# Optimization experiments

Measured on AMD Instinct MI355X. Metric: run time of the kernel, lower is better.

## Reference

```python
import jax, jax.numpy as jnp
import numpy as np

UNITS, D_IN, K_CONN, BATCH = 1024, 2048, 16, 4096
TEMP = 1.0  # temperature_update_tf at step=0 (epoch 0)
EPS = 1e-20


def setup_inputs() -> dict:
    key = jax.random.key(0)
    kx, kw, kd, kg = jax.random.split(key, 4)
    x = jax.random.normal(kx, (BATCH, D_IN), dtype=jnp.float32)
    # he_uniform for W
    limit = np.sqrt(6.0 / D_IN).astype(np.float32)
    W = jax.random.uniform(kw, (UNITS, D_IN), minval=-limit, maxval=limit, dtype=jnp.float32)
    # logits D ~ N(0, 0.5)
    D = 0.5 * jax.random.normal(kd, (UNITS, D_IN), dtype=jnp.float32)
    # Gumbel noise, scaled by -0.001 as in the original (BS=1)
    u = jax.random.uniform(kg, (1, UNITS, D_IN), dtype=jnp.float32)
    GN = -0.001 * jnp.log(-jnp.log(u + EPS) + EPS)
    return {"x": x, "W": W, "D": D, "GN": GN, "k": K_CONN}


def _hard_sigmoid(v):
    return jnp.clip(0.2 * v + 0.5, 0.0, 1.0)


def reference(x, W, D, GN, k):
    logits = D  # [units, d]
    perturbed = logits[None, :, :] + GN  # [1, units, d]
    # top-k indices, then sorted ascending (TF: top_k of indices + reverse)
    _, idx = jax.lax.top_k(perturbed, k)           # [1, units, k]
    idx_sorted = jnp.sort(idx, axis=-1)             # ascending index order
    hard = jax.nn.one_hot(idx_sorted, D_IN, dtype=perturbed.dtype)  # [1, units, k, d]
    # exclusive cumsum over the k axis
    cum = jnp.cumsum(hard, axis=-2) - hard
    # softmax((log(exp(logits)*(1-cum+eps)) + GN)/Temp) == softmax((logits + log(1-cum+eps) + GN)/Temp)
    scores = (logits[None, :, None, :] + jnp.log(1.0 - cum + EPS) + GN[:, :, None, :]) / TEMP
    soft = jax.nn.softmax(scores, axis=-1)          # [1, units, k, d]
    samples = jax.lax.stop_gradient(hard - soft) + soft
    A = samples.sum(axis=-2).sum(axis=0)            # [units, d]
    # straight-through binary weights
    w_soft = 2.0 * _hard_sigmoid(W) - 1.0
    w_bin = jax.lax.stop_gradient(jnp.sign(W) - w_soft) + w_soft
    AW = A * w_bin                                   # [units, d]
    y = x @ AW.T                                     # [batch, units]
    return y
```

## Files before the change

kernel.cpp:

```cpp
#include <hip/hip_runtime.h>
#include <hip/hip_bf16.h>

#define UNITS 1024
#define DIN   2048
#define KCONN 16
#define BATCH 4096
#define BB    8

__global__ __launch_bounds__(256) void topk_sel_kernel(
    const float* __restrict__ Dl, const float* __restrict__ GN,
    const float* __restrict__ W, int* __restrict__ selCi,
    float* __restrict__ selC) {
  __shared__ float P[4][DIN];
  __shared__ int chosen[4][KCONN];
  const int lane = threadIdx.x & 63;
  const int wv   = threadIdx.x >> 6;
  const int u    = blockIdx.x * 4 + wv;

  const float4* D4 = (const float4*)(Dl + (size_t)u * DIN);
  const float4* G4 = (const float4*)(GN + (size_t)u * DIN);
  float4* P4 = (float4*)P[wv];
#pragma unroll
  for (int i = 0; i < DIN / 4 / 64; ++i) {
    int e = i * 64 + lane;
    float4 d = D4[e], g = G4[e];
    P4[e] = make_float4(d.x + g.x, d.y + g.y, d.z + g.z, d.w + g.w);
  }
  __syncthreads();

  for (int it = 0; it < KCONN; ++it) {
    float best = -INFINITY;
    int   bi   = 0;
#pragma unroll
    for (int i = 0; i < DIN / 64; ++i) {
      float v = P[wv][i * 64 + lane];
      if (v > best) { best = v; bi = i * 64 + lane; }
    }
    unsigned b  = __float_as_uint(best);
    unsigned kv = b ^ (((int)b < 0) ? 0xFFFFFFFFu : 0x80000000u);
    int id = bi;
#define DSTEP(CTRL, RM) { \
    unsigned kv2 = (unsigned)__builtin_amdgcn_update_dpp((int)kv, (int)kv, CTRL, RM, 0xF, false); \
    int id2 = __builtin_amdgcn_update_dpp(id, id, CTRL, RM, 0xF, false); \
    bool tk = (kv2 > kv) || ((kv2 == kv) && (id2 < id)); \
    kv = tk ? kv2 : kv; id = tk ? id2 : id; }
    DSTEP(0x111, 0xF)
    DSTEP(0x112, 0xF)
    DSTEP(0x114, 0xF)
    DSTEP(0x118, 0xF)
    DSTEP(0x142, 0xA)
    DSTEP(0x143, 0xC)
#undef DSTEP
    int widx = __builtin_amdgcn_readlane(id, 63);
    if (lane == (widx & 63)) P[wv][widx] = -INFINITY;
    if (lane == 0) chosen[wv][it] = widx;
  }

  if (lane < KCONN) {
    int gi = chosen[wv][lane];
    float w = W[(size_t)u * DIN + gi];
    float c = (w > 0.0f) ? 1.0f : ((w < 0.0f) ? -1.0f : 0.0f);
    selCi[u * KCONN + lane] = gi ^ ((gi >> 3) & 7);
    selC[u * KCONN + lane]  = c;
  }
}

__global__ __launch_bounds__(512) void gather_mm_kernel(
    const float* __restrict__ x, const int* __restrict__ selCi,
    const float* __restrict__ selC, float* __restrict__ y) {
  __shared__ uint4 xs[DIN];
  const int t = threadIdx.x;
  const size_t b0 = (size_t)blockIdx.x * BB;

  const int4*   Ia = (const int4*)(selCi + t * KCONN);
  const int4*   Ib = (const int4*)(selCi + (t + 512) * KCONN);
  const float4* Ca = (const float4*)(selC + t * KCONN);
  const float4* Cb = (const float4*)(selC + (t + 512) * KCONN);
  int4   i0 = Ia[0], i1 = Ia[1], i2 = Ia[2], i3 = Ia[3];
  int4   i4 = Ib[0], i5 = Ib[1], i6 = Ib[2], i7 = Ib[3];
  float4 c0 = Ca[0], c1 = Ca[1], c2 = Ca[2], c3 = Ca[3];
  float4 c4 = Cb[0], c5 = Cb[1], c6 = Cb[2], c7 = Cb[3];

  const float* xb = x + b0 * DIN + 4 * t;
  float4 r0 = *(const float4*)(xb + 0 * DIN);
  float4 r1 = *(const float4*)(xb + 1 * DIN);
  float4 r2 = *(const float4*)(xb + 2 * DIN);
  float4 r3 = *(const float4*)(xb + 3 * DIN);
  float4 r4 = *(const float4*)(xb + 4 * DIN);
  float4 r5 = *(const float4*)(xb + 5 * DIN);
  float4 r6 = *(const float4*)(xb + 6 * DIN);
  float4 r7 = *(const float4*)(xb + 7 * DIN);

#define PK2(LO, HI) ({ __hip_bfloat16 l_ = __float2bfloat16(LO), h_ = __float2bfloat16(HI); \
  (unsigned)(*(unsigned short*)&l_) | ((unsigned)(*(unsigned short*)&h_) << 16); })
#define MKCH(J, C) { const int d_ = 4 * t + (J); const int sd_ = d_ ^ ((d_ >> 3) & 7); \
  uint4 ch_; ch_.x = PK2(r0.C, r1.C); ch_.y = PK2(r2.C, r3.C); \
  ch_.z = PK2(r4.C, r5.C); ch_.w = PK2(r6.C, r7.C); xs[sd_] = ch_; }
  MKCH(0, x) MKCH(1, y) MKCH(2, z) MKCH(3, w)
#undef MKCH
#undef PK2
  __syncthreads();

#define BL(w) __uint_as_float((w) << 16)
#define BH(w) __uint_as_float((w) & 0xffff0000u)
#define GJ(CI, CC) { uint4 v_ = xs[CI]; const float cc_ = (CC); \
  a0 = fmaf(cc_, BL(v_.x), a0); a1 = fmaf(cc_, BH(v_.x), a1); \
  a2 = fmaf(cc_, BL(v_.y), a2); a3 = fmaf(cc_, BH(v_.y), a3); \
  a4 = fmaf(cc_, BL(v_.z), a4); a5 = fmaf(cc_, BH(v_.z), a5); \
  a6 = fmaf(cc_, BL(v_.w), a6); a7 = fmaf(cc_, BH(v_.w), a7); }
#define UNIT(IA, IB, IC, ID, CA, CB, CC_, CD, U) { \
  float a0 = 0, a1 = 0, a2 = 0, a3 = 0, a4 = 0, a5 = 0, a6 = 0, a7 = 0; \
  GJ(IA.x, CA.x) GJ(IA.y, CA.y) GJ(IA.z, CA.z) GJ(IA.w, CA.w) \
  GJ(IB.x, CB.x) GJ(IB.y, CB.y) GJ(IB.z, CB.z) GJ(IB.w, CB.w) \
  GJ(IC.x, CC_.x) GJ(IC.y, CC_.y) GJ(IC.z, CC_.z) GJ(IC.w, CC_.w) \
  GJ(ID.x, CD.x) GJ(ID.y, CD.y) GJ(ID.z, CD.z) GJ(ID.w, CD.w) \
  const int u_ = (U); \
  y[(b0 + 0) * UNITS + u_] = a0; y[(b0 + 1) * UNITS + u_] = a1; \
  y[(b0 + 2) * UNITS + u_] = a2; y[(b0 + 3) * UNITS + u_] = a3; \
  y[(b0 + 4) * UNITS + u_] = a4; y[(b0 + 5) * UNITS + u_] = a5; \
  y[(b0 + 6) * UNITS + u_] = a6; y[(b0 + 7) * UNITS + u_] = a7; }

  UNIT(i0, i1, i2, i3, c0, c1, c2, c3, t)
  UNIT(i4, i5, i6, i7, c4, c5, c6, c7, t + 512)
#undef UNIT
#undef GJ
#undef BL
#undef BH
}

extern "C" void kernel_launch(void* const* d_in, const int* in_sizes, int n_in,
                              void* d_out, int out_size, void* d_ws, size_t ws_size,
                              hipStream_t stream) {
  const float* x  = (const float*)d_in[0];
  const float* W  = (const float*)d_in[1];
  const float* Dl = (const float*)d_in[2];
  const float* GN = (const float*)d_in[3];
  float* y = (float*)d_out;

  int*   selCi = (int*)d_ws;
  float* selC  = (float*)((char*)d_ws + UNITS * KCONN * sizeof(int));

  topk_sel_kernel<<<UNITS / 4, 256, 0, stream>>>(Dl, GN, W, selCi, selC);
  gather_mm_kernel<<<BATCH / BB, 512, 0, stream>>>(x, selCi, selC, y);
}
```

Before: 32.71 us.

## Register-resident top-k with per-lane top-2 cache and sign-packed gather indices

The top-k kernel now keeps each lane's 32 perturbed logits in registers and caches a per-lane top-2. This replaces the per-iteration full LDS rescan, and a lane only rescans its registers when both cached candidates are consumed. The selection output packs the swizzled column index and the sign bit of W into one int, with a zero-row sentinel for w==0. The gather kernel therefore loads half the metadata and applies the sign by XOR instead of an FMA. Nontemporal loads and stores are added for the streamed x, D, GN and y traffic.

```diff
diff --git a/kernel.cpp b/kernel.cpp
--- a/kernel.cpp
+++ b/kernel.cpp
@@ -7,43 +7,60 @@
 #define BATCH 4096
 #define BB    8
 
+typedef float    f32x4 __attribute__((ext_vector_type(4)));
+typedef unsigned u32x4 __attribute__((ext_vector_type(4)));
+typedef int      i32x4 __attribute__((ext_vector_type(4)));
+
+#define LDNT4F(P) __builtin_nontemporal_load((const f32x4*)(P))
+
 __global__ __launch_bounds__(256) void topk_sel_kernel(
     const float* __restrict__ Dl, const float* __restrict__ GN,
-    const float* __restrict__ W, int* __restrict__ selCi,
-    float* __restrict__ selC) {
-  __shared__ float P[4][DIN];
-  __shared__ int chosen[4][KCONN];
+    const float* __restrict__ W, int* __restrict__ selP) {
   const int lane = threadIdx.x & 63;
   const int wv   = threadIdx.x >> 6;
   const int u    = blockIdx.x * 4 + wv;
 
-  const float4* D4 = (const float4*)(Dl + (size_t)u * DIN);
-  const float4* G4 = (const float4*)(GN + (size_t)u * DIN);
-  float4* P4 = (float4*)P[wv];
+  const f32x4* D4 = (const f32x4*)(Dl + (size_t)u * DIN);
+  const f32x4* G4 = (const f32x4*)(GN + (size_t)u * DIN);
+  float v[32];
 #pragma unroll
-  for (int i = 0; i < DIN / 4 / 64; ++i) {
-    int e = i * 64 + lane;
-    float4 d = D4[e], g = G4[e];
-    P4[e] = make_float4(d.x + g.x, d.y + g.y, d.z + g.z, d.w + g.w);
+  for (int i4 = 0; i4 < 8; ++i4) {
+    f32x4 d = LDNT4F(D4 + i4 * 64 + lane);
+    f32x4 g = LDNT4F(G4 + i4 * 64 + lane);
+    v[i4 * 4 + 0] = d[0] + g[0];
+    v[i4 * 4 + 1] = d[1] + g[1];
+    v[i4 * 4 + 2] = d[2] + g[2];
+    v[i4 * 4 + 3] = d[3] + g[3];
   }
-  __syncthreads();
 
+  float m1 = -INFINITY, m2 = -INFINITY;
+  int   l1 = 0, l2 = 0;
+#pragma unroll
+  for (int l = 0; l < 32; ++l) {
+    float xv = v[l];
+    bool g1t = xv > m1;
+    bool g2t = xv > m2;
+    m2 = g1t ? m1 : (g2t ? xv : m2);
+    l2 = g1t ? l1 : (g2t ? l : l2);
+    m1 = g1t ? xv : m1;
+    l1 = g1t ? l  : l1;
+  }
+
+  unsigned claimed = 0;
+  int navail = 2;
+  int gsel = 0;
+
+#pragma unroll 1
   for (int it = 0; it < KCONN; ++it) {
-    float best = -INFINITY;
-    int   bi   = 0;
-#pragma unroll
-    for (int i = 0; i < DIN / 64; ++i) {
-      float v = P[wv][i * 64 + lane];
-      if (v > best) { best = v; bi = i * 64 + lane; }
-    }
-    unsigned b  = __float_as_uint(best);
-    unsigned kv = b ^ (((int)b < 0) ? 0xFFFFFFFFu : 0x80000000u);
-    int id = bi;
+    unsigned kb = __float_as_uint(m1);
+    unsigned kv = kb ^ (((int)kb < 0) ? 0xFFFFFFFFu : 0x80000000u);
+    int g1 = ((l1 >> 2) << 8) | (lane << 2) | (l1 & 3);
+    unsigned rk = kv; int rg = g1;
 #define DSTEP(CTRL, RM) { \
-    unsigned kv2 = (unsigned)__builtin_amdgcn_update_dpp((int)kv, (int)kv, CTRL, RM, 0xF, false); \
-    int id2 = __builtin_amdgcn_update_dpp(id, id, CTRL, RM, 0xF, false); \
-    bool tk = (kv2 > kv) || ((kv2 == kv) && (id2 < id)); \
-    kv = tk ? kv2 : kv; id = tk ? id2 : id; }
+    unsigned k2_ = (unsigned)__builtin_amdgcn_update_dpp((int)rk, (int)rk, CTRL, RM, 0xF, false); \
+    int g2_ = __builtin_amdgcn_update_dpp(rg, rg, CTRL, RM, 0xF, false); \
+    bool tk_ = (k2_ > rk) || ((k2_ == rk) && (g2_ < rg)); \
+    rk = tk_ ? k2_ : rk; rg = tk_ ? g2_ : rg; }
     DSTEP(0x111, 0xF)
     DSTEP(0x112, 0xF)
     DSTEP(0x114, 0xF)
@@ -51,81 +68,102 @@
     DSTEP(0x142, 0xA)
     DSTEP(0x143, 0xC)
 #undef DSTEP
-    int widx = __builtin_amdgcn_readlane(id, 63);
-    if (lane == (widx & 63)) P[wv][widx] = -INFINITY;
-    if (lane == 0) chosen[wv][it] = widx;
+    int wg = __builtin_amdgcn_readlane(rg, 63);
+    if (lane == it) gsel = wg;
+
+    bool own  = (g1 == wg);
+    bool need = own && (navail == 1);
+    if (own) claimed |= 1u << l1;
+    if (own && navail == 2) { m1 = m2; l1 = l2; navail = 1; }
+    if (need) {
+      float bm = -INFINITY; int bl = 0;
+#pragma unroll
+      for (int l = 0; l < 32; ++l) {
+        float xv = (claimed & (1u << l)) ? -INFINITY : v[l];
+        if (xv > bm) { bm = xv; bl = l; }
+      }
+      m1 = bm; l1 = bl;
+    }
   }
 
   if (lane < KCONN) {
-    int gi = chosen[wv][lane];
-    float w = W[(size_t)u * DIN + gi];
-    float c = (w > 0.0f) ? 1.0f : ((w < 0.0f) ? -1.0f : 0.0f);
-    selCi[u * KCONN + lane] = gi ^ ((gi >> 3) & 7);
-    selC[u * KCONN + lane]  = c;
+    int g = gsel;
+    float w = W[(size_t)u * DIN + g];
+    int sd = g ^ ((g >> 3) & 7);
+    int pa = (w == 0.0f) ? (DIN << 1)
+                         : ((sd << 1) | (w < 0.0f ? 1 : 0));
+    selP[u * KCONN + lane] = pa;
   }
 }
 
 __global__ __launch_bounds__(512) void gather_mm_kernel(
-    const float* __restrict__ x, const int* __restrict__ selCi,
-    const float* __restrict__ selC, float* __restrict__ y) {
-  __shared__ uint4 xs[DIN];
+    const float* __restrict__ x, const int* __restrict__ selP,
+    float* __restrict__ y) {
+  __shared__ u32x4 xs[DIN + 1];
   const int t = threadIdx.x;
   const size_t b0 = (size_t)blockIdx.x * BB;
 
-  const int4*   Ia = (const int4*)(selCi + t * KCONN);
-  const int4*   Ib = (const int4*)(selCi + (t + 512) * KCONN);
-  const float4* Ca = (const float4*)(selC + t * KCONN);
-  const float4* Cb = (const float4*)(selC + (t + 512) * KCONN);
-  int4   i0 = Ia[0], i1 = Ia[1], i2 = Ia[2], i3 = Ia[3];
-  int4   i4 = Ib[0], i5 = Ib[1], i6 = Ib[2], i7 = Ib[3];
-  float4 c0 = Ca[0], c1 = Ca[1], c2 = Ca[2], c3 = Ca[3];
-  float4 c4 = Cb[0], c5 = Cb[1], c6 = Cb[2], c7 = Cb[3];
+  const i32x4* S0 = (const i32x4*)(selP + t * KCONN);
+  const i32x4* S1 = (const i32x4*)(selP + (t + 512) * KCONN);
+  i32x4 sA0 = S0[0], sA1 = S0[1], sA2 = S0[2], sA3 = S0[3];
+  i32x4 sB0 = S1[0], sB1 = S1[1], sB2 = S1[2], sB3 = S1[3];
 
   const float* xb = x + b0 * DIN + 4 * t;
-  float4 r0 = *(const float4*)(xb + 0 * DIN);
-  float4 r1 = *(const float4*)(xb + 1 * DIN);
-  float4 r2 = *(const float4*)(xb + 2 * DIN);
-  float4 r3 = *(const float4*)(xb + 3 * DIN);
-  float4 r4 = *(const float4*)(xb + 4 * DIN);
-  float4 r5 = *(const float4*)(xb + 5 * DIN);
-  float4 r6 = *(const float4*)(xb + 6 * DIN);
-  float4 r7 = *(const float4*)(xb + 7 * DIN);
+  f32x4 r0 = LDNT4F(xb + 0 * DIN);
+  f32x4 r1 = LDNT4F(xb + 1 * DIN);
+  f32x4 r2 = LDNT4F(xb + 2 * DIN);
+  f32x4 r3 = LDNT4F(xb + 3 * DIN);
+  f32x4 r4 = LDNT4F(xb + 4 * DIN);
+  f32x4 r5 = LDNT4F(xb + 5 * DIN);
+  f32x4 r6 = LDNT4F(xb + 6 * DIN);
+  f32x4 r7 = LDNT4F(xb + 7 * DIN);
 
 #define PK2(LO, HI) ({ __hip_bfloat16 l_ = __float2bfloat16(LO), h_ = __float2bfloat16(HI); \
   (unsigned)(*(unsigned short*)&l_) | ((unsigned)(*(unsigned short*)&h_) << 16); })
-#define MKCH(J, C) { const int d_ = 4 * t + (J); const int sd_ = d_ ^ ((d_ >> 3) & 7); \
-  uint4 ch_; ch_.x = PK2(r0.C, r1.C); ch_.y = PK2(r2.C, r3.C); \
-  ch_.z = PK2(r4.C, r5.C); ch_.w = PK2(r6.C, r7.C); xs[sd_] = ch_; }
-  MKCH(0, x) MKCH(1, y) MKCH(2, z) MKCH(3, w)
-#undef MKCH
+#pragma unroll
+  for (int j = 0; j < 4; ++j) {
+    const int d  = 4 * t + j;
+    const int sd = d ^ ((d >> 3) & 7);
+    u32x4 ch;
+    ch[0] = PK2(r0[j], r1[j]);
+    ch[1] = PK2(r2[j], r3[j]);
+    ch[2] = PK2(r4[j], r5[j]);
+    ch[3] = PK2(r6[j], r7[j]);
+    xs[sd] = ch;
+  }
 #undef PK2
+  if (t == 0) { u32x4 z = {0, 0, 0, 0}; xs[DIN] = z; }
   __syncthreads();
 
-#define BL(w) __uint_as_float((w) << 16)
-#define BH(w) __uint_as_float((w) & 0xffff0000u)
-#define GJ(CI, CC) { uint4 v_ = xs[CI]; const float cc_ = (CC); \
-  a0 = fmaf(cc_, BL(v_.x), a0); a1 = fmaf(cc_, BH(v_.x), a1); \
-  a2 = fmaf(cc_, BL(v_.y), a2); a3 = fmaf(cc_, BH(v_.y), a3); \
-  a4 = fmaf(cc_, BL(v_.z), a4); a5 = fmaf(cc_, BH(v_.z), a5); \
-  a6 = fmaf(cc_, BL(v_.w), a6); a7 = fmaf(cc_, BH(v_.w), a7); }
-#define UNIT(IA, IB, IC, ID, CA, CB, CC_, CD, U) { \
+#define GJ(PA) { unsigned pa_ = (unsigned)(PA); \
+  u32x4 vv_ = xs[pa_ >> 1]; \
+  unsigned sm_ = (pa_ & 1u) ? 0x80008000u : 0u; \
+  vv_[0] ^= sm_; vv_[1] ^= sm_; vv_[2] ^= sm_; vv_[3] ^= sm_; \
+  a0 += __uint_as_float(vv_[0] << 16); a1 += __uint_as_float(vv_[0] & 0xffff0000u); \
+  a2 += __uint_as_float(vv_[1] << 16); a3 += __uint_as_float(vv_[1] & 0xffff0000u); \
+  a4 += __uint_as_float(vv_[2] << 16); a5 += __uint_as_float(vv_[2] & 0xffff0000u); \
+  a6 += __uint_as_float(vv_[3] << 16); a7 += __uint_as_float(vv_[3] & 0xffff0000u); }
+
+#define UNIT(SA, SB, SC, SD, U) { \
   float a0 = 0, a1 = 0, a2 = 0, a3 = 0, a4 = 0, a5 = 0, a6 = 0, a7 = 0; \
-  GJ(IA.x, CA.x) GJ(IA.y, CA.y) GJ(IA.z, CA.z) GJ(IA.w, CA.w) \
-  GJ(IB.x, CB.x) GJ(IB.y, CB.y) GJ(IB.z, CB.z) GJ(IB.w, CB.w) \
-  GJ(IC.x, CC_.x) GJ(IC.y, CC_.y) GJ(IC.z, CC_.z) GJ(IC.w, CC_.w) \
-  GJ(ID.x, CD.x) GJ(ID.y, CD.y) GJ(ID.z, CD.z) GJ(ID.w, CD.w) \
+  GJ(SA[0]) GJ(SA[1]) GJ(SA[2]) GJ(SA[3]) \
+  GJ(SB[0]) GJ(SB[1]) GJ(SB[2]) GJ(SB[3]) \
+  GJ(SC[0]) GJ(SC[1]) GJ(SC[2]) GJ(SC[3]) \
+  GJ(SD[0]) GJ(SD[1]) GJ(SD[2]) GJ(SD[3]) \
   const int u_ = (U); \
-  y[(b0 + 0) * UNITS + u_] = a0; y[(b0 + 1) * UNITS + u_] = a1; \
-  y[(b0 + 2) * UNITS + u_] = a2; y[(b0 + 3) * UNITS + u_] = a3; \
-  y[(b0 + 4) * UNITS + u_] = a4; y[(b0 + 5) * UNITS + u_] = a5; \
-  y[(b0 + 6) * UNITS + u_] = a6; y[(b0 + 7) * UNITS + u_] = a7; }
+  __builtin_nontemporal_store(a0, &y[(b0 + 0) * UNITS + u_]); \
+  __builtin_nontemporal_store(a1, &y[(b0 + 1) * UNITS + u_]); \
+  __builtin_nontemporal_store(a2, &y[(b0 + 2) * UNITS + u_]); \
+  __builtin_nontemporal_store(a3, &y[(b0 + 3) * UNITS + u_]); \
+  __builtin_nontemporal_store(a4, &y[(b0 + 4) * UNITS + u_]); \
+  __builtin_nontemporal_store(a5, &y[(b0 + 5) * UNITS + u_]); \
+  __builtin_nontemporal_store(a6, &y[(b0 + 6) * UNITS + u_]); \
+  __builtin_nontemporal_store(a7, &y[(b0 + 7) * UNITS + u_]); }
 
-  UNIT(i0, i1, i2, i3, c0, c1, c2, c3, t)
-  UNIT(i4, i5, i6, i7, c4, c5, c6, c7, t + 512)
+  UNIT(sA0, sA1, sA2, sA3, t)
+  UNIT(sB0, sB1, sB2, sB3, t + 512)
 #undef UNIT
 #undef GJ
-#undef BL
-#undef BH
 }
 
 extern "C" void kernel_launch(void* const* d_in, const int* in_sizes, int n_in,
@@ -137,9 +175,8 @@
   const float* GN = (const float*)d_in[3];
   float* y = (float*)d_out;
 
-  int*   selCi = (int*)d_ws;
-  float* selC  = (float*)((char*)d_ws + UNITS * KCONN * sizeof(int));
+  int* selP = (int*)d_ws;
 
-  topk_sel_kernel<<<UNITS / 4, 256, 0, stream>>>(Dl, GN, W, selCi, selC);
-  gather_mm_kernel<<<BATCH / BB, 512, 0, stream>>>(x, selCi, selC, y);
+  topk_sel_kernel<<<UNITS / 4, 256, 0, stream>>>(Dl, GN, W, selP);
+  gather_mm_kernel<<<BATCH / BB, 512, 0, stream>>>(x, selP, y);
 }
```

After: 26.50 us, median of 2. 19.0% less time.
